# Kernel optimization log

Hardware: AMD Instinct MI355X
Metric: run time of the kernel (lower is better)

The kernel has to match this reference:

```python
import jax, jax.numpy as jnp
import numpy as np

GROUPS = 8
EPS = 1e-5


def setup_inputs() -> dict:
    key = jax.random.key(0)
    k1, k2, k3 = jax.random.split(key, 3)
    B, C, H, W = 4, 256, 64, 64
    x = jax.random.normal(k1, (B, C, H, W), dtype=jnp.float32)
    gamma = jnp.ones((C,), dtype=jnp.float32)
    beta = jnp.zeros((C,), dtype=jnp.float32)
    # conv1x1 weights flattened to [out, in]
    w_qkv = jax.random.normal(k2, (3 * C, C), dtype=jnp.float32) * (C ** -0.5)
    w_proj = jax.random.normal(k3, (C, C), dtype=jnp.float32) * (C ** -0.5)
    b_proj = jnp.zeros((C,), dtype=jnp.float32)
    return {"x": x, "gamma": gamma, "beta": beta, "w_qkv": w_qkv,
            "w_proj": w_proj, "b_proj": b_proj}


def group_norm(x, gamma, beta):
    B, C, H, W = x.shape
    xr = x.reshape(B, GROUPS, C // GROUPS, H * W)
    mu = xr.mean(axis=(2, 3), keepdims=True)
    var = xr.var(axis=(2, 3), keepdims=True)
    xn = (xr - mu) * jax.lax.rsqrt(var + EPS)
    xn = xn.reshape(B, C, H * W)
    return xn * gamma[None, :, None] + beta[None, :, None]


def reference(x, gamma, beta, w_qkv, w_proj, b_proj):
    B, C, H, W = x.shape
    N = H * W
    xn = group_norm(x, gamma, beta)               # [B, C, N]
    qkv = jnp.einsum('oc,bcn->bon', w_qkv, xn)    # [B, 3C, N]
    q, k, v = jnp.split(qkv, 3, axis=1)           # each [B, C, N]
    # attn[b, n, m] = sum_c q[b,c,n] * k[b,c,m] * C^-0.5
    scores = jnp.einsum('bcn,bcm->bnm', q, k) * (C ** -0.5)  # [B, N, N]
    attn = jax.nn.softmax(scores, axis=-1)
    # out = v @ attn^T  -> out[b,c,n] = sum_m v[b,c,m] * attn[b,n,m]
    out = jnp.einsum('bcm,bnm->bcn', v, attn)     # [B, C, N]
    y = jnp.einsum('oc,bcn->bon', w_proj, out) + b_proj[None, :, None]
    return x + y.reshape(B, C, H, W)
```

## Files before the change

### kernel.cpp

```cpp
#include <hip/hip_runtime.h>
#include <hip/hip_bf16.h>

#define BB 4
#define CC 256
#define NN 4096
#define GG 8
#define SPLITS 4
#define TKV 64
#define ITERS (NN / SPLITS / TKV)

typedef unsigned char u8;
typedef unsigned short u16;
typedef unsigned int u32;
typedef __bf16 b16x8 __attribute__((ext_vector_type(8)));
typedef float f32x4 __attribute__((ext_vector_type(4)));
typedef u32 u32x4 __attribute__((ext_vector_type(4)));
typedef u32 u32x2 __attribute__((ext_vector_type(2)));
typedef u16 u16x4 __attribute__((ext_vector_type(4)));

#define QS 0.09016844005556021f
#define FMAX 8.0f


__device__ __forceinline__ u16 f2bf(float f) {
    u32 u = __builtin_bit_cast(u32, f);
    u = (u + 0x7FFFu + ((u >> 16) & 1u)) >> 16;
    return (u16)u;
}

__device__ __forceinline__ float bf2f(u16 h) {
    return __builtin_bit_cast(float, (u32)h << 16);
}

__device__ __forceinline__ u32 pack_bf2(float a, float b) {
    float2 f; f.x = a; f.y = b;
    __hip_bfloat162 h = __float22bfloat162_rn(f);
    u32 r;
    __builtin_memcpy(&r, &h, 4);
    return r;
}

__device__ __forceinline__ float exp2_raw(float x) {
#if __has_builtin(__builtin_amdgcn_exp2f)
    return __builtin_amdgcn_exp2f(x);
#else
    float r;
    asm("v_exp_f32 %0, %1" : "=v"(r) : "v"(x));
    return r;
#endif
}

__device__ __forceinline__ b16x8 ldfrag(const u16* p) {
    u32x4 v = *reinterpret_cast<const u32x4*>(p);
    return __builtin_bit_cast(b16x8, v);
}

__device__ __forceinline__ int pk_fp8x4(float a, float b, float c, float d) {
    int r = __builtin_amdgcn_cvt_pk_fp8_f32(a, b, 0, false);
    r = __builtin_amdgcn_cvt_pk_fp8_f32(c, d, r, true);
    return r;
}

__device__ __forceinline__ long as_long(u32x2 v) { return __builtin_bit_cast(long, v); }

typedef __attribute__((address_space(1))) const unsigned int* gas_p;
typedef __attribute__((address_space(3))) unsigned int* las_p;

__device__ __forceinline__ void g2l(const u8* g, u8* l) {
    __builtin_amdgcn_global_load_lds((gas_p)g, (las_p)l, 16, 0, 0);
}

__device__ __forceinline__ void g2l16(const u16* g, u16* l) {
    __builtin_amdgcn_global_load_lds((gas_p)g, (las_p)l, 16, 0, 0);
}

__global__ void fold_w(const float* __restrict__ w_qkv, const float* __restrict__ w_proj,
                       const float* __restrict__ gamma, const float* __restrict__ beta,
                       const float* __restrict__ stats,
                       u16* __restrict__ wqf, float* __restrict__ biasq,
                       u16* __restrict__ wpf) {
    int o = blockIdx.x;
    int b = blockIdx.y;
    int c = threadIdx.x;
    int g = c >> 5;
    float mu   = stats[(b * GG + g) * 2];
    float rstd = stats[(b * GG + g) * 2 + 1];
    float a  = gamma[c] * rstd;
    float bb = beta[c] - mu * a;
    float w = w_qkv[o * CC + c];
    size_t fe = ((size_t)((o >> 4) * 8 + (c >> 5)) * 64 + ((c & 31) >> 3) * 16 + (o & 15)) * 8 + (c & 7);
    wqf[(size_t)b * 768 * CC + fe] = f2bf(w * a);
    float part = w * bb;
    #pragma unroll
    for (int off = 32; off; off >>= 1) part += __shfl_down(part, off, 64);
    __shared__ float red[4];
    if ((threadIdx.x & 63) == 0) red[threadIdx.x >> 6] = part;
    __syncthreads();
    if (threadIdx.x == 0) biasq[b * 768 + o] = red[0] + red[1] + red[2] + red[3];
    if (b == 0 && o < CC) {
        float wp = w_proj[o * CC + c];
        wpf[fe] = f2bf(wp);
    }
}

__global__ void transpose_x(const float* __restrict__ x, u16* __restrict__ xtf,
                            float* __restrict__ gsum) {
    __shared__ float tile[64][65];
    __shared__ float red[4][4];
    int n0 = blockIdx.x * 64, c0 = blockIdx.y * 64, b = blockIdx.z;
    int t = threadIdx.x;
    int col = t & 63, r0 = t >> 6;
    const float* xp = x + (size_t)b * CC * NN;
    float s0 = 0.f, ss0 = 0.f, s1 = 0.f, ss1 = 0.f;
    #pragma unroll
    for (int i = 0; i < 16; ++i) {
        int row = i * 4 + r0;
        float v = xp[(size_t)(c0 + row) * NN + n0 + col];
        tile[row][col] = v;
        if (i < 8) { s0 += v; ss0 += v * v; } else { s1 += v; ss1 += v * v; }
    }
    #pragma unroll
    for (int off = 32; off; off >>= 1) {
        s0 += __shfl_down(s0, off, 64); ss0 += __shfl_down(ss0, off, 64);
        s1 += __shfl_down(s1, off, 64); ss1 += __shfl_down(ss1, off, 64);
    }
    int wid = t >> 6;
    if ((t & 63) == 0) { red[wid][0] = s0; red[wid][1] = ss0; red[wid][2] = s1; red[wid][3] = ss1; }
    __syncthreads();
    if (t < 2) {
        float s  = red[0][t * 2] + red[1][t * 2] + red[2][t * 2] + red[3][t * 2];
        float ss = red[0][t * 2 + 1] + red[1][t * 2 + 1] + red[2][t * 2 + 1] + red[3][t * 2 + 1];
        int g = (c0 >> 5) + t;
        atomicAdd(&gsum[(b * GG + g) * 2], s);
        atomicAdd(&gsum[(b * GG + g) * 2 + 1], ss);
    }
    int nl = t >> 2;
    int cbq = t & 3;
    int l15 = nl & 15;
    int ntile = (n0 >> 4) + (nl >> 4);
    int kk = (c0 >> 5) + (cbq >> 1);
    u16* ob = xtf + (size_t)b * NN * CC;
    #pragma unroll
    for (int g = 0; g < 4; ++g) {
        int quad = (cbq & 1) * 2 + (g >> 1);
        int j0 = (g & 1) * 4;
        u16x4 v;
        v.x = f2bf(tile[cbq * 16 + g * 4 + 0][nl]);
        v.y = f2bf(tile[cbq * 16 + g * 4 + 1][nl]);
        v.z = f2bf(tile[cbq * 16 + g * 4 + 2][nl]);
        v.w = f2bf(tile[cbq * 16 + g * 4 + 3][nl]);
        *reinterpret_cast<u16x4*>(ob + ((size_t)(ntile * 8 + kk) * 64 + quad * 16 + l15) * 8 + j0) = v;
    }
}

__global__ void gn_finalize(const float* __restrict__ gsum, float* __restrict__ stats) {
    int i = threadIdx.x;
    if (i < BB * GG) {
        float s = gsum[i * 2], ss = gsum[i * 2 + 1];
        const float inv = 1.f / ((CC / GG) * NN);
        float mu = s * inv;
        float var = ss * inv - mu * mu;
        stats[i * 2] = mu;
        stats[i * 2 + 1] = rsqrtf(var + 1e-5f);
    }
}

__global__ void __launch_bounds__(256) qkv_gemm(const u16* __restrict__ wqf,
                                                const float* __restrict__ biasq,
                                                const u16* __restrict__ xtf,
                                                u8* __restrict__ qtf, u8* __restrict__ ktf,
                                                u8* __restrict__ vvf) {
    __shared__ u16 bx[16384];
    int b = blockIdx.z;
    int o0 = blockIdx.y * 128;
    int n0 = blockIdx.x * 64;
    int lane = threadIdx.x & 63, w = threadIdx.x >> 6;
    int l15 = lane & 15, quad = lane >> 4;
    const u16* Bg = xtf + (size_t)b * NN * CC + (size_t)n0 * 256;
    #pragma unroll
    for (int j = 0; j < 8; ++j) {
        int c = w * 8 + j;
        g2l16(Bg + (size_t)c * 512 + lane * 8, bx + (size_t)c * 512 + lane * 8);
    }
    __syncthreads();

    const u16* A = wqf + (size_t)b * 768 * CC;
    f32x4 acc[2][4] = {};
    #pragma unroll
    for (int kk = 0; kk < 8; ++kk) {
        b16x8 af[2];
        #pragma unroll
        for (int t = 0; t < 2; ++t) {
            int otile = (o0 >> 4) + w * 2 + t;
            af[t] = ldfrag(A + (size_t)(otile * 8 + kk) * 512 + lane * 8);
        }
        #pragma unroll
        for (int nt = 0; nt < 4; ++nt) {
            b16x8 bf = ldfrag(bx + (size_t)(nt * 8 + kk) * 512 + lane * 8);
            acc[0][nt] = __builtin_amdgcn_mfma_f32_16x16x32_bf16(af[0], bf, acc[0][nt], 0, 0, 0);
            acc[1][nt] = __builtin_amdgcn_mfma_f32_16x16x32_bf16(af[1], bf, acc[1][nt], 0, 0, 0);
        }
    }
    #pragma unroll
    for (int t = 0; t < 2; ++t) {
        int o_base = o0 + (w * 2 + t) * 16 + quad * 4;
        float bias[4];
        #pragma unroll
        for (int r = 0; r < 4; ++r) bias[r] = biasq[b * 768 + o_base + r];
        if (o0 < 512) {
            int oloc = (o0 < 256) ? o_base : (o_base - 256);
            u8* dst = ((o0 < 256) ? qtf : ktf) + (size_t)b * NN * CC;
            #pragma unroll
            for (int nt = 0; nt < 4; ++nt) {
                int n = n0 + nt * 16 + l15;
                int pk = pk_fp8x4(acc[t][nt][0] + bias[0], acc[t][nt][1] + bias[1],
                                  acc[t][nt][2] + bias[2], acc[t][nt][3] + bias[3]);
                size_t addr = (size_t)((n >> 4) * 4 + (oloc >> 6)) * 1024
                            + ((oloc & 31) >> 3) * 256 + (n & 15) * 16
                            + ((oloc >> 5) & 1) * 8 + (oloc & 7);
                *reinterpret_cast<u32*>(dst + addr) = (u32)pk;
            }
        } else {
            int cb = o_base - 512;
            u8* dst = vvf + (size_t)b * NN * CC;
            #pragma unroll
            for (int nt = 0; nt < 4; ++nt) {
                int kv = n0 + nt * 16 + l15;
                int pk = pk_fp8x4(acc[t][nt][0] + bias[0], acc[t][nt][1] + bias[1],
                                  acc[t][nt][2] + bias[2], acc[t][nt][3] + bias[3]);
                size_t base = (size_t)((kv >> 5) * 8 + (cb >> 5)) * 1024
                            + ((kv & 31) >> 3) * 256 + ((cb >> 4) & 1) * 8 + (kv & 7);
                #pragma unroll
                for (int r = 0; r < 4; ++r)
                    dst[base + ((cb & 15) + r) * 16] = (u8)(pk >> (r * 8));
            }
        }
    }
}

__global__ void __launch_bounds__(512, 4) flash(const u8* __restrict__ qtf,
                                                const u8* __restrict__ ktf,
                                                const u8* __restrict__ vvf,
                                                u16* __restrict__ po,
                                                float* __restrict__ lp) {
    __shared__ u8 kbuf[2][16384];
    __shared__ u8 vbuf[2][16384];
    __shared__ u8 pbuf[8][16 * 72];
    int lin = blockIdx.x;
    int chunk = lin & 15;
    int nblk = lin >> 4;
    int b = chunk >> 2, sp = chunk & 3;
    int lane = threadIdx.x & 63, w = threadIdx.x >> 6;
    int l15 = lane & 15, quad = lane >> 4;
    int ntile = nblk * 8 + w;
    const u8* kb8 = ktf + (size_t)b * NN * CC;
    const u8* vb8 = vvf + (size_t)b * NN * CC;
    u8* pw = &pbuf[w][0];

    const u32x2 ones2 = {0x38383838u, 0x38383838u};
    const long ones8 = as_long(ones2);

    u32x4 aq[4];
    const u8* qb = qtf + (size_t)b * NN * CC + (size_t)ntile * 4096;
    #pragma unroll
    for (int s = 0; s < 4; ++s)
        aq[s] = *reinterpret_cast<const u32x4*>(qb + s * 1024 + lane * 16);

    f32x4 acco[16] = {};
    f32x4 acco_l = {};

    const int m_beg = sp * (NN / SPLITS);

    auto stage = [&](int buf, int m0) {
        const u8* ks = kb8 + ((size_t)m0 << 8);
        const u8* vs = vb8 + ((size_t)m0 << 8);
        #pragma unroll
        for (int j = 0; j < 4; ++j) {
            int idx = w * 4 + j;
            if (idx < 16) g2l(ks + idx * 1024 + lane * 16, &kbuf[buf][idx * 1024]);
            else          g2l(vs + (idx - 16) * 1024 + lane * 16, &vbuf[buf][(idx - 16) * 1024]);
        }
    };

    stage(0, m_beg);
    __syncthreads();
    for (int it = 0; it < ITERS; ++it) {
        int cur = it & 1;
        if (it + 1 < ITERS) stage(cur ^ 1, m_beg + (it + 1) * TKV);
        const u8* kc = &kbuf[cur][0];
        const u8* vc = &vbuf[cur][0];
        f32x4 accs[4] = {};
        #pragma unroll
        for (int s = 0; s < 4; ++s) {
            long alo = as_long(u32x2{aq[s].x, aq[s].y});
            long ahi = as_long(u32x2{aq[s].z, aq[s].w});
            #pragma unroll
            for (int m = 0; m < 4; ++m) {
                u32x4 kf = *reinterpret_cast<const u32x4*>(kc + (size_t)(m * 4 + s) * 1024 + lane * 16);
                accs[m] = __builtin_amdgcn_mfma_f32_16x16x32_fp8_fp8(
                    alo, as_long(u32x2{kf.x, kf.y}), accs[m], 0, 0, 0);
                accs[m] = __builtin_amdgcn_mfma_f32_16x16x32_fp8_fp8(
                    ahi, as_long(u32x2{kf.z, kf.w}), accs[m], 0, 0, 0);
            }
        }
        #pragma unroll
        for (int m = 0; m < 4; ++m) {
            float e0 = exp2_raw(fmaf(accs[m][0], QS, -FMAX));
            float e1 = exp2_raw(fmaf(accs[m][1], QS, -FMAX));
            float e2 = exp2_raw(fmaf(accs[m][2], QS, -FMAX));
            float e3 = exp2_raw(fmaf(accs[m][3], QS, -FMAX));
            int p01 = __builtin_amdgcn_cvt_pk_fp8_f32(e0, e1, 0, false);
            int p23 = __builtin_amdgcn_cvt_pk_fp8_f32(e2, e3, 0, false);
            u8* pr = pw + m * 16 + l15;
            pr[(quad * 4 + 0) * 72] = (u8)p01;
            pr[(quad * 4 + 1) * 72] = (u8)(p01 >> 8);
            pr[(quad * 4 + 2) * 72] = (u8)p23;
            pr[(quad * 4 + 3) * 72] = (u8)(p23 >> 8);
        }
        asm volatile("s_waitcnt lgkmcnt(0)" ::: "memory");
        long ap0 = as_long(*reinterpret_cast<const u32x2*>(pw + l15 * 72 + quad * 8));
        long ap1 = as_long(*reinterpret_cast<const u32x2*>(pw + l15 * 72 + 32 + quad * 8));
        acco_l = __builtin_amdgcn_mfma_f32_16x16x32_fp8_fp8(ap0, ones8, acco_l, 0, 0, 0);
        acco_l = __builtin_amdgcn_mfma_f32_16x16x32_fp8_fp8(ap1, ones8, acco_l, 0, 0, 0);
        #pragma unroll
        for (int c2 = 0; c2 < 8; ++c2) {
            u32x4 vf0 = *reinterpret_cast<const u32x4*>(vc + (size_t)c2 * 1024 + lane * 16);
            u32x4 vf1 = *reinterpret_cast<const u32x4*>(vc + (size_t)(8 + c2) * 1024 + lane * 16);
            acco[c2 * 2]     = __builtin_amdgcn_mfma_f32_16x16x32_fp8_fp8(
                ap0, as_long(u32x2{vf0.x, vf0.y}), acco[c2 * 2], 0, 0, 0);
            acco[c2 * 2 + 1] = __builtin_amdgcn_mfma_f32_16x16x32_fp8_fp8(
                ap0, as_long(u32x2{vf0.z, vf0.w}), acco[c2 * 2 + 1], 0, 0, 0);
            acco[c2 * 2]     = __builtin_amdgcn_mfma_f32_16x16x32_fp8_fp8(
                ap1, as_long(u32x2{vf1.x, vf1.y}), acco[c2 * 2], 0, 0, 0);
            acco[c2 * 2 + 1] = __builtin_amdgcn_mfma_f32_16x16x32_fp8_fp8(
                ap1, as_long(u32x2{vf1.z, vf1.w}), acco[c2 * 2 + 1], 0, 0, 0);
        }
        __syncthreads();
    }
    u16* pochunk = po + ((size_t)(sp * BB + b) * 256 + ntile) * 4096;
    #pragma unroll
    for (int ct = 0; ct < 16; ++ct) {
        u32x2 st;
        st.x = pack_bf2(acco[ct][0], acco[ct][1]);
        st.y = pack_bf2(acco[ct][2], acco[ct][3]);
        *reinterpret_cast<u32x2*>(pochunk + (size_t)(ct * 64 + quad * 16 + l15) * 4) = st;
    }
    if (l15 == 0) {
        size_t lbase = (size_t)(sp * BB + b) * NN + ntile * 16;
        #pragma unroll
        for (int r = 0; r < 4; ++r) lp[lbase + quad * 4 + r] = acco_l[r];
    }
}

__global__ void __launch_bounds__(256) combine(const u16* __restrict__ po,
                                               const float* __restrict__ lp,
                                               u16* __restrict__ otf) {
    int idx = blockIdx.x * 256 + threadIdx.x;
    int cg   = idx & 31;
    int quad = (idx >> 5) & 3;
    int nb   = (idx >> 7) & 255;
    int b    = idx >> 15;
    float acc[4][8] = {};
    float lsum[4] = {};
    #pragma unroll
    for (int s = 0; s < SPLITS; ++s) {
        const u16* src = po + (((size_t)(s * BB + b) * 256 + nb) * 4096)
                       + ((cg >> 1) * 256 + quad * 64 + (cg & 1) * 32);
        u16 s16[32];
        #pragma unroll
        for (int q = 0; q < 4; ++q)
            *reinterpret_cast<u32x4*>(&s16[q * 8]) = *reinterpret_cast<const u32x4*>(src + q * 8);
        #pragma unroll
        for (int r = 0; r < 4; ++r)
            #pragma unroll
            for (int j = 0; j < 8; ++j)
                acc[r][j] += bf2f(s16[j * 4 + r]);
        #pragma unroll
        for (int r = 0; r < 4; ++r)
            lsum[r] += lp[(size_t)(s * BB + b) * NN + nb * 16 + quad * 4 + r];
    }
    u16* dstb = otf + (size_t)b * NN * CC;
    #pragma unroll
    for (int r = 0; r < 4; ++r) {
        float inv = 1.f / lsum[r];
        u16 outv[8];
        #pragma unroll
        for (int j = 0; j < 8; ++j) outv[j] = f2bf(acc[r][j] * inv);
        size_t off = ((size_t)(nb * 8 + (cg >> 2)) * 64 + (cg & 3) * 16 + quad * 4 + r) * 8;
        *reinterpret_cast<u32x4*>(dstb + off) = *reinterpret_cast<const u32x4*>(outv);
    }
}

__global__ void __launch_bounds__(256) proj(const u16* __restrict__ wpf,
                                            const float* __restrict__ b_proj,
                                            const u16* __restrict__ otf,
                                            const float* __restrict__ x,
                                            float* __restrict__ out) {
    int b = blockIdx.z, o0 = blockIdx.y * 64, n0 = blockIdx.x * 64;
    int lane = threadIdx.x & 63, w = threadIdx.x >> 6;
    int l15 = lane & 15, quad = lane >> 4;
    const u16* Bp = otf + (size_t)b * NN * CC;
    int otile = (o0 >> 4) + w;
    f32x4 acc[4] = {};
    #pragma unroll
    for (int kk = 0; kk < 8; ++kk) {
        b16x8 af = ldfrag(wpf + (size_t)(otile * 8 + kk) * 512 + lane * 8);
        #pragma unroll
        for (int nt = 0; nt < 4; ++nt) {
            b16x8 bf = ldfrag(Bp + (size_t)(((n0 >> 4) + nt) * 8 + kk) * 512 + lane * 8);
            acc[nt] = __builtin_amdgcn_mfma_f32_16x16x32_bf16(af, bf, acc[nt], 0, 0, 0);
        }
    }
    int o_base = o0 + w * 16 + quad * 4;
    #pragma unroll
    for (int nt = 0; nt < 4; ++nt) {
        int n = n0 + nt * 16 + l15;
        #pragma unroll
        for (int r = 0; r < 4; ++r) {
            int o = o_base + r;
            size_t idx = ((size_t)(b * CC + o)) * NN + n;
            out[idx] = acc[nt][r] + b_proj[o] + x[idx];
        }
    }
}

extern "C" void kernel_launch(void* const* d_in, const int* in_sizes, int n_in,
                              void* d_out, int out_size, void* d_ws, size_t ws_size,
                              hipStream_t stream) {
    const float* x      = (const float*)d_in[0];
    const float* gamma  = (const float*)d_in[1];
    const float* beta   = (const float*)d_in[2];
    const float* w_qkv  = (const float*)d_in[3];
    const float* w_proj = (const float*)d_in[4];
    const float* b_proj = (const float*)d_in[5];
    float* out = (float*)d_out;

    char* p = (char*)d_ws;
    float* stats = (float*)p; p += 256;
    float* gsum  = (float*)p; p += 256;
    float* biasq = (float*)p; p += (size_t)BB * 768 * sizeof(float);
    u16* wqf = (u16*)p; p += (size_t)BB * 768 * CC * 2;
    u16* wpf = (u16*)p; p += (size_t)CC * CC * 2;
    u16* xtf = (u16*)p; p += (size_t)BB * NN * CC * 2;
    u8* qtf8 = (u8*)p; p += (size_t)BB * NN * CC;
    u8* ktf8 = (u8*)p; p += (size_t)BB * NN * CC;
    u8* vvf8 = (u8*)p; p += (size_t)BB * NN * CC;
    u16* otf = (u16*)p; p += (size_t)BB * NN * CC * 2;
    u16* po = (u16*)p; p += (size_t)SPLITS * BB * NN * CC * 2;
    float* lp = (float*)p; p += (size_t)SPLITS * BB * NN * sizeof(float);
    (void)ws_size; (void)in_sizes; (void)n_in; (void)out_size;

    (void)hipMemsetAsync(gsum, 0, BB * GG * 2 * sizeof(float), stream);
    transpose_x<<<dim3(NN / 64, CC / 64, BB), 256, 0, stream>>>(x, xtf, gsum);
    gn_finalize<<<1, 64, 0, stream>>>(gsum, stats);
    fold_w<<<dim3(768, BB), 256, 0, stream>>>(w_qkv, w_proj, gamma, beta, stats, wqf, biasq, wpf);
    qkv_gemm<<<dim3(NN / 64, 6, BB), 256, 0, stream>>>(wqf, biasq, xtf, qtf8, ktf8, vvf8);
    flash<<<(NN / 128) * SPLITS * BB, 512, 0, stream>>>(qtf8, ktf8, vvf8, po, lp);
    combine<<<(BB * NN * CC / 32) / 256, 256, 0, stream>>>(po, lp, otf);
    proj<<<dim3(NN / 64, CC / 64, BB), 256, 0, stream>>>(wpf, b_proj, otf, x, out);
}
```

Before: 185.0 us.

## Fuse split-combine into projection GEMM and fold GN finalize into weight folding

Merges the split-KV combine step into the projection kernel: each 512-thread block reduces the partial outputs for its 64 tokens into LDS as bf16 fragments, then runs the projection MFMAs over all 256 output channels from LDS. This removes the otf global round trip and one launch. The gn_finalize kernel is dropped, and each fold_w thread recomputes mean and rstd from the raw sums. transpose_x now reads x with float4 loads. The trade-off is a grid of only 256 proj blocks, which lowers parallelism, and the combine reads are no longer spread across many small blocks.

```diff
diff --git a/kernel.cpp b/kernel.cpp
--- a/kernel.cpp
+++ b/kernel.cpp
@@ -76,15 +76,18 @@
 
 __global__ void fold_w(const float* __restrict__ w_qkv, const float* __restrict__ w_proj,
                        const float* __restrict__ gamma, const float* __restrict__ beta,
-                       const float* __restrict__ stats,
+                       const float* __restrict__ gsum,
                        u16* __restrict__ wqf, float* __restrict__ biasq,
                        u16* __restrict__ wpf) {
     int o = blockIdx.x;
     int b = blockIdx.y;
     int c = threadIdx.x;
     int g = c >> 5;
-    float mu   = stats[(b * GG + g) * 2];
-    float rstd = stats[(b * GG + g) * 2 + 1];
+    const float inv = 1.f / ((CC / GG) * NN);
+    float s  = gsum[(b * GG + g) * 2];
+    float ss = gsum[(b * GG + g) * 2 + 1];
+    float mu = s * inv;
+    float rstd = rsqrtf(ss * inv - mu * mu + 1e-5f);
     float a  = gamma[c] * rstd;
     float bb = beta[c] - mu * a;
     float w = w_qkv[o * CC + c];
@@ -109,15 +112,19 @@
     __shared__ float red[4][4];
     int n0 = blockIdx.x * 64, c0 = blockIdx.y * 64, b = blockIdx.z;
     int t = threadIdx.x;
-    int col = t & 63, r0 = t >> 6;
+    int c4 = (t & 15) * 4;
+    int r0 = t >> 4;
     const float* xp = x + (size_t)b * CC * NN;
     float s0 = 0.f, ss0 = 0.f, s1 = 0.f, ss1 = 0.f;
     #pragma unroll
-    for (int i = 0; i < 16; ++i) {
-        int row = i * 4 + r0;
-        float v = xp[(size_t)(c0 + row) * NN + n0 + col];
-        tile[row][col] = v;
-        if (i < 8) { s0 += v; ss0 += v * v; } else { s1 += v; ss1 += v * v; }
+    for (int i = 0; i < 4; ++i) {
+        int row = i * 16 + r0;
+        float4 v = *reinterpret_cast<const float4*>(&xp[(size_t)(c0 + row) * NN + n0 + c4]);
+        tile[row][c4 + 0] = v.x; tile[row][c4 + 1] = v.y;
+        tile[row][c4 + 2] = v.z; tile[row][c4 + 3] = v.w;
+        float s = v.x + v.y + v.z + v.w;
+        float q = v.x * v.x + v.y * v.y + v.z * v.z + v.w * v.w;
+        if (i < 2) { s0 += s; ss0 += q; } else { s1 += s; ss1 += q; }
     }
     #pragma unroll
     for (int off = 32; off; off >>= 1) {
@@ -150,18 +157,6 @@
         v.z = f2bf(tile[cbq * 16 + g * 4 + 2][nl]);
         v.w = f2bf(tile[cbq * 16 + g * 4 + 3][nl]);
         *reinterpret_cast<u16x4*>(ob + ((size_t)(ntile * 8 + kk) * 64 + quad * 16 + l15) * 8 + j0) = v;
-    }
-}
-
-__global__ void gn_finalize(const float* __restrict__ gsum, float* __restrict__ stats) {
-    int i = threadIdx.x;
-    if (i < BB * GG) {
-        float s = gsum[i * 2], ss = gsum[i * 2 + 1];
-        const float inv = 1.f / ((CC / GG) * NN);
-        float mu = s * inv;
-        float var = ss * inv - mu * mu;
-        stats[i * 2] = mu;
-        stats[i * 2 + 1] = rsqrtf(var + 1e-5f);
     }
 }
 
@@ -352,74 +347,78 @@
     }
 }
 
-__global__ void __launch_bounds__(256) combine(const u16* __restrict__ po,
-                                               const float* __restrict__ lp,
-                                               u16* __restrict__ otf) {
-    int idx = blockIdx.x * 256 + threadIdx.x;
-    int cg   = idx & 31;
-    int quad = (idx >> 5) & 3;
-    int nb   = (idx >> 7) & 255;
-    int b    = idx >> 15;
-    float acc[4][8] = {};
-    float lsum[4] = {};
-    #pragma unroll
-    for (int s = 0; s < SPLITS; ++s) {
-        const u16* src = po + (((size_t)(s * BB + b) * 256 + nb) * 4096)
-                       + ((cg >> 1) * 256 + quad * 64 + (cg & 1) * 32);
-        u16 s16[32];
-        #pragma unroll
-        for (int q = 0; q < 4; ++q)
-            *reinterpret_cast<u32x4*>(&s16[q * 8]) = *reinterpret_cast<const u32x4*>(src + q * 8);
-        #pragma unroll
-        for (int r = 0; r < 4; ++r)
-            #pragma unroll
-            for (int j = 0; j < 8; ++j)
-                acc[r][j] += bf2f(s16[j * 4 + r]);
-        #pragma unroll
-        for (int r = 0; r < 4; ++r)
-            lsum[r] += lp[(size_t)(s * BB + b) * NN + nb * 16 + quad * 4 + r];
-    }
-    u16* dstb = otf + (size_t)b * NN * CC;
-    #pragma unroll
-    for (int r = 0; r < 4; ++r) {
-        float inv = 1.f / lsum[r];
-        u16 outv[8];
-        #pragma unroll
-        for (int j = 0; j < 8; ++j) outv[j] = f2bf(acc[r][j] * inv);
-        size_t off = ((size_t)(nb * 8 + (cg >> 2)) * 64 + (cg & 3) * 16 + quad * 4 + r) * 8;
-        *reinterpret_cast<u32x4*>(dstb + off) = *reinterpret_cast<const u32x4*>(outv);
-    }
-}
-
-__global__ void __launch_bounds__(256) proj(const u16* __restrict__ wpf,
+__global__ void __launch_bounds__(512) proj(const u16* __restrict__ wpf,
                                             const float* __restrict__ b_proj,
-                                            const u16* __restrict__ otf,
+                                            const u16* __restrict__ po,
+                                            const float* __restrict__ lp,
                                             const float* __restrict__ x,
                                             float* __restrict__ out) {
-    int b = blockIdx.z, o0 = blockIdx.y * 64, n0 = blockIdx.x * 64;
-    int lane = threadIdx.x & 63, w = threadIdx.x >> 6;
+    __shared__ u16 bO[16384];
+    int b = blockIdx.y, n0 = blockIdx.x * 64;
+    int t = threadIdx.x;
+    {
+        int cg = t & 31, quad = (t >> 5) & 3, ntl = t >> 7;
+        int nb = (n0 >> 4) + ntl;
+        float acc[4][8] = {};
+        float lsum[4] = {};
+        #pragma unroll
+        for (int s = 0; s < SPLITS; ++s) {
+            const u16* src = po + (((size_t)(s * BB + b) * 256 + nb) * 4096)
+                           + ((cg >> 1) * 256 + quad * 64 + (cg & 1) * 32);
+            u16 s16[32];
+            #pragma unroll
+            for (int q = 0; q < 4; ++q)
+                *reinterpret_cast<u32x4*>(&s16[q * 8]) = *reinterpret_cast<const u32x4*>(src + q * 8);
+            #pragma unroll
+            for (int r = 0; r < 4; ++r)
+                #pragma unroll
+                for (int j = 0; j < 8; ++j)
+                    acc[r][j] += bf2f(s16[j * 4 + r]);
+            #pragma unroll
+            for (int r = 0; r < 4; ++r)
+                lsum[r] += lp[(size_t)(s * BB + b) * NN + nb * 16 + quad * 4 + r];
+        }
+        #pragma unroll
+        for (int r = 0; r < 4; ++r) {
+            float inv = 1.f / lsum[r];
+            u16 outv[8];
+            #pragma unroll
+            for (int j = 0; j < 8; ++j) outv[j] = f2bf(acc[r][j] * inv);
+            size_t off = ((size_t)(ntl * 8 + (cg >> 2)) * 64 + (cg & 3) * 16 + quad * 4 + r) * 8;
+            *reinterpret_cast<u32x4*>(bO + off) = *reinterpret_cast<const u32x4*>(outv);
+        }
+    }
+    __syncthreads();
+    int lane = t & 63, w = t >> 6;
     int l15 = lane & 15, quad = lane >> 4;
-    const u16* Bp = otf + (size_t)b * NN * CC;
-    int otile = (o0 >> 4) + w;
-    f32x4 acc[4] = {};
+    f32x4 acc2[2][4] = {};
     #pragma unroll
     for (int kk = 0; kk < 8; ++kk) {
-        b16x8 af = ldfrag(wpf + (size_t)(otile * 8 + kk) * 512 + lane * 8);
+        b16x8 af[2];
+        #pragma unroll
+        for (int tt = 0; tt < 2; ++tt) {
+            int otile = w * 2 + tt;
+            af[tt] = ldfrag(wpf + (size_t)(otile * 8 + kk) * 512 + lane * 8);
+        }
         #pragma unroll
         for (int nt = 0; nt < 4; ++nt) {
-            b16x8 bf = ldfrag(Bp + (size_t)(((n0 >> 4) + nt) * 8 + kk) * 512 + lane * 8);
-            acc[nt] = __builtin_amdgcn_mfma_f32_16x16x32_bf16(af, bf, acc[nt], 0, 0, 0);
-        }
-    }
-    int o_base = o0 + w * 16 + quad * 4;
-    #pragma unroll
-    for (int nt = 0; nt < 4; ++nt) {
-        int n = n0 + nt * 16 + l15;
-        #pragma unroll
-        for (int r = 0; r < 4; ++r) {
-            int o = o_base + r;
-            size_t idx = ((size_t)(b * CC + o)) * NN + n;
-            out[idx] = acc[nt][r] + b_proj[o] + x[idx];
+            b16x8 bf = ldfrag(bO + (size_t)(nt * 8 + kk) * 512 + lane * 8);
+            acc2[0][nt] = __builtin_amdgcn_mfma_f32_16x16x32_bf16(af[0], bf, acc2[0][nt], 0, 0, 0);
+            acc2[1][nt] = __builtin_amdgcn_mfma_f32_16x16x32_bf16(af[1], bf, acc2[1][nt], 0, 0, 0);
+        }
+    }
+    #pragma unroll
+    for (int tt = 0; tt < 2; ++tt) {
+        int o_base = (w * 2 + tt) * 16 + quad * 4;
+        #pragma unroll
+        for (int nt = 0; nt < 4; ++nt) {
+            int n = n0 + nt * 16 + l15;
+            #pragma unroll
+            for (int r = 0; r < 4; ++r) {
+                int o = o_base + r;
+                size_t idx = ((size_t)(b * CC + o)) * NN + n;
+                out[idx] = acc2[tt][nt][r] + b_proj[o] + x[idx];
+            }
         }
     }
 }
@@ -436,7 +435,6 @@
     float* out = (float*)d_out;
 
     char* p = (char*)d_ws;
-    float* stats = (float*)p; p += 256;
     float* gsum  = (float*)p; p += 256;
     float* biasq = (float*)p; p += (size_t)BB * 768 * sizeof(float);
     u16* wqf = (u16*)p; p += (size_t)BB * 768 * CC * 2;
@@ -445,17 +443,14 @@
     u8* qtf8 = (u8*)p; p += (size_t)BB * NN * CC;
     u8* ktf8 = (u8*)p; p += (size_t)BB * NN * CC;
     u8* vvf8 = (u8*)p; p += (size_t)BB * NN * CC;
-    u16* otf = (u16*)p; p += (size_t)BB * NN * CC * 2;
     u16* po = (u16*)p; p += (size_t)SPLITS * BB * NN * CC * 2;
     float* lp = (float*)p; p += (size_t)SPLITS * BB * NN * sizeof(float);
     (void)ws_size; (void)in_sizes; (void)n_in; (void)out_size;
 
     (void)hipMemsetAsync(gsum, 0, BB * GG * 2 * sizeof(float), stream);
     transpose_x<<<dim3(NN / 64, CC / 64, BB), 256, 0, stream>>>(x, xtf, gsum);
-    gn_finalize<<<1, 64, 0, stream>>>(gsum, stats);
-    fold_w<<<dim3(768, BB), 256, 0, stream>>>(w_qkv, w_proj, gamma, beta, stats, wqf, biasq, wpf);
+    fold_w<<<dim3(768, BB), 256, 0, stream>>>(w_qkv, w_proj, gamma, beta, gsum, wqf, biasq, wpf);
     qkv_gemm<<<dim3(NN / 64, 6, BB), 256, 0, stream>>>(wqf, biasq, xtf, qtf8, ktf8, vvf8);
     flash<<<(NN / 128) * SPLITS * BB, 512, 0, stream>>>(qtf8, ktf8, vvf8, po, lp);
-    combine<<<(BB * NN * CC / 32) / 256, 256, 0, stream>>>(po, lp, otf);
-    proj<<<dim3(NN / 64, CC / 64, BB), 256, 0, stream>>>(wpf, b_proj, otf, x, out);
-}
+    proj<<<dim3(NN / 64, BB), 512, 0, stream>>>(wpf, b_proj, po, lp, x, out);
+}
```

Result: faster. 172.4 us (-6.8%).
